# Kernel tuning notes

Measured on AMD Instinct MI355X. Metric: run time of the kernel, lower is better.

## Reference

```python
import jax, jax.numpy as jnp
import numpy as np

TOP_K = 2  # num_experts_per_tok


def setup_inputs() -> dict:
    B, L, D, F, E = 4, 2048, 1024, 2048, 8
    key = jax.random.key(0)
    k0, k1, k2, k3, k4 = jax.random.split(key, 5)
    x = jax.random.normal(k0, (B, L, D), jnp.float32)
    gate_w = jax.random.normal(k1, (D, E), jnp.float32) * 0.02   # router Linear (no bias)
    w1 = jax.random.normal(k2, (E, D, F), jnp.float32) * 0.02    # expert gate proj
    w3 = jax.random.normal(k3, (E, D, F), jnp.float32) * 0.02    # expert up proj
    w2 = jax.random.normal(k4, (E, F, D), jnp.float32) * 0.02    # expert down proj
    return {"x": x, "gate_w": gate_w, "w1": w1, "w3": w3, "w2": w2}


def reference(x, gate_w, w1, w3, w2):
    # ep_size=1: the all_to_all dispatch/return are identities; the math reduces to
    # topk routing -> softmax over selected logits -> per-expert SwiGLU -> weighted combine.
    B, L, D = x.shape
    E = w1.shape[0]
    xf = x.reshape(-1, D)                                  # [N, D]
    N = xf.shape[0]
    router_logits = xf @ gate_w                            # [N, E]
    topk_w, topk_i = jax.lax.top_k(router_logits.astype(jnp.float32), TOP_K)
    topk_w = jax.nn.softmax(topk_w, axis=-1).astype(x.dtype)  # [N, K]
    # Scatter top-k weights into a dense per-expert combine weight [N, E]
    comb = jnp.zeros((N, E), x.dtype)
    comb = comb.at[jnp.arange(N)[:, None], topk_i].add(topk_w)
    # Grouped expert compute: loop over the small fixed expert set, mask-combine.
    out = jnp.zeros_like(xf)
    for e in range(E):
        h = jax.nn.silu(xf @ w1[e]) * (xf @ w3[e])         # [N, F] SwiGLU
        out = out + comb[:, e:e + 1] * (h @ w2[e])         # weighted index_add combine
    return out.reshape(B, L, D), router_logits
```

## Files before the change

### kernel.cpp

```cpp
#include <hip/hip_runtime.h>
#include <hip/hip_bf16.h>

#define DEV __device__ __forceinline__

typedef __attribute__((ext_vector_type(8))) short short8;
typedef __attribute__((ext_vector_type(4))) float f32x4;

constexpr int NTOK = 8192;
constexpr int DIM  = 1024;
constexpr int FF   = 2048;
constexpr int NE   = 8;
constexpr int BM = 128, BN = 128, BK = 64;

DEV void async_copy16(const void* g, void* l) {
  __builtin_amdgcn_global_load_lds(
      (const __attribute__((address_space(1))) unsigned int*)g,
      (__attribute__((address_space(3))) unsigned int*)l, 16, 0, 0);
}

DEV float silu_f(float v) { return v / (1.f + __expf(-v)); }

__global__ void k_convx(const float* __restrict__ x, __hip_bfloat16* __restrict__ xb) {
  size_t i = (size_t)blockIdx.x * blockDim.x + threadIdx.x;
  const float4* s = (const float4*)x + i * 2;
  float4 a = s[0], b = s[1];
  __hip_bfloat16 tmp[8];
  tmp[0] = __float2bfloat16(a.x); tmp[1] = __float2bfloat16(a.y);
  tmp[2] = __float2bfloat16(a.z); tmp[3] = __float2bfloat16(a.w);
  tmp[4] = __float2bfloat16(b.x); tmp[5] = __float2bfloat16(b.y);
  tmp[6] = __float2bfloat16(b.z); tmp[7] = __float2bfloat16(b.w);
  *(short8*)(xb + i * 8) = *(const short8*)tmp;
}

__global__ void k_tconv(const float* __restrict__ src, __hip_bfloat16* __restrict__ dst,
                        int R, int C) {
  const size_t esz = (size_t)R * C;
  src += esz * blockIdx.z;
  dst += esz * blockIdx.z;
  __shared__ float tile[32][33];
  const int t = threadIdx.x;
  const int r0 = blockIdx.y * 32, c0 = blockIdx.x * 32;
#pragma unroll
  for (int i = 0; i < 4; ++i) {
    int lr = i * 8 + (t >> 5), lc = t & 31;
    tile[lr][lc] = src[(size_t)(r0 + lr) * C + c0 + lc];
  }
  __syncthreads();
#pragma unroll
  for (int i = 0; i < 4; ++i) {
    int cc = i * 8 + (t >> 5), rr = t & 31;
    dst[(size_t)(c0 + cc) * R + r0 + rr] = __float2bfloat16(tile[rr][cc]);
  }
}

__global__ void k_router(const float* __restrict__ x, const float* __restrict__ gw,
                         float* __restrict__ logits, int* __restrict__ tok_i,
                         float2* __restrict__ tok_w) {
  const int wave = threadIdx.x >> 6, lane = threadIdx.x & 63;
  const int tok = blockIdx.x * 4 + wave;
  float acc[NE];
#pragma unroll
  for (int e = 0; e < NE; ++e) acc[e] = 0.f;
  const float4* xr = (const float4*)(x + (size_t)tok * DIM);
#pragma unroll
  for (int i = 0; i < DIM / 256; ++i) {
    int d4 = i * 64 + lane;
    float4 xv = xr[d4];
    const float4* g = (const float4*)(gw + (size_t)d4 * 4 * NE);
    float xs[4] = {xv.x, xv.y, xv.z, xv.w};
#pragma unroll
    for (int r = 0; r < 4; ++r) {
      float4 ga = g[r * 2], gb = g[r * 2 + 1];
      acc[0] += xs[r] * ga.x; acc[1] += xs[r] * ga.y;
      acc[2] += xs[r] * ga.z; acc[3] += xs[r] * ga.w;
      acc[4] += xs[r] * gb.x; acc[5] += xs[r] * gb.y;
      acc[6] += xs[r] * gb.z; acc[7] += xs[r] * gb.w;
    }
  }
#pragma unroll
  for (int e = 0; e < NE; ++e) {
#pragma unroll
    for (int off = 32; off; off >>= 1) acc[e] += __shfl_xor(acc[e], off);
  }
  if (lane == 0) {
#pragma unroll
    for (int e = 0; e < NE; ++e) logits[(size_t)tok * NE + e] = acc[e];
    int i0 = 0; float m0 = acc[0];
#pragma unroll
    for (int e = 1; e < NE; ++e) if (acc[e] > m0) { m0 = acc[e]; i0 = e; }
    int i1 = -1; float m1 = -3.4e38f;
#pragma unroll
    for (int e = 0; e < NE; ++e) if (e != i0 && acc[e] > m1) { m1 = acc[e]; i1 = e; }
    float p  = __expf(m1 - m0);
    float wA = 1.f / (1.f + p);
    float wB = p * wA;
    tok_i[tok] = i0 | (i1 << 4);
    tok_w[tok] = make_float2(wA, wB);
  }
}

__global__ void k_place(const int* __restrict__ tok_i, const float2* __restrict__ tok_w,
                        int* __restrict__ slot_token, float* __restrict__ slot_w,
                        int* __restrict__ counts) {
  __shared__ int lcnt[NE], lbase[NE];
  const int t = threadIdx.x;
  const int tok = blockIdx.x * 256 + t;
  if (t < NE) lcnt[t] = 0;
  __syncthreads();
  int pk = tok_i[tok];
  int e0 = pk & 15, e1 = pk >> 4;
  float2 w = tok_w[tok];
  int p0 = atomicAdd(&lcnt[e0], 1);
  int p1 = atomicAdd(&lcnt[e1], 1);
  __syncthreads();
  if (t < NE) lbase[t] = atomicAdd(&counts[t], lcnt[t]);
  __syncthreads();
  int s0 = e0 * NTOK + lbase[e0] + p0;
  slot_token[s0] = tok; slot_w[s0] = w.x;
  int s1 = e1 * NTOK + lbase[e1] + p1;
  slot_token[s1] = tok; slot_w[s1] = w.y;
}

__global__ void k_scan(const int* __restrict__ counts, int* __restrict__ offsets) {
  if (threadIdx.x == 0) {
    int s = 0;
    for (int e = 0; e < NE; ++e) { offsets[e] = s; s += counts[e]; }
  }
}

__global__ __launch_bounds__(256, 2) void k_expert_up(
    const __hip_bfloat16* __restrict__ xb,
    const __hip_bfloat16* __restrict__ w1t,
    const __hip_bfloat16* __restrict__ w3t,
    const int* __restrict__ slot_token, const int* __restrict__ counts,
    const int* __restrict__ offsets,
    __hip_bfloat16* __restrict__ h)
{
  const int e  = blockIdx.z;
  const int cnt = counts[e];
  const int m0 = blockIdx.y * BM;
  if (m0 >= cnt) return;
  const int n0 = blockIdx.x * BN;
  const int tid = threadIdx.x, lane = tid & 63, wave = tid >> 6;
  const int wrow = (wave >> 1) * 64, wcol = (wave & 1) * 64;

  __shared__ __hip_bfloat16 sA[BM * BK];
  __shared__ __hip_bfloat16 sB1[BN * BK];
  __shared__ __hip_bfloat16 sB3[BN * BK];

  const int srow = tid >> 3, scol = tid & 7;
  const int swz = scol ^ (srow & 7);

  const int* stok = slot_token + e * NTOK;
  const __hip_bfloat16* b1e = w1t + (size_t)e * FF * DIM;
  const __hip_bfloat16* b3e = w3t + (size_t)e * FF * DIM;

  const __hip_bfloat16 *gA[4], *gB1[4], *gB3[4];
#pragma unroll
  for (int i = 0; i < 4; ++i) {
    int r = i * 32 + srow;
    int idx = m0 + r;
    int tokv = (idx < cnt) ? stok[idx] : 0;
    gA[i]  = xb  + (size_t)tokv * DIM + swz * 8;
    gB1[i] = b1e + (size_t)(n0 + r) * DIM + swz * 8;
    gB3[i] = b3e + (size_t)(n0 + r) * DIM + swz * 8;
  }
  char* dA  = (char*)sA  + tid * 16;
  char* dB1 = (char*)sB1 + tid * 16;
  char* dB3 = (char*)sB3 + tid * 16;

  f32x4 acc1[4][4], acc3[4][4];
#pragma unroll
  for (int m = 0; m < 4; ++m)
#pragma unroll
    for (int n = 0; n < 4; ++n) { acc1[m][n] = {0, 0, 0, 0}; acc3[m][n] = {0, 0, 0, 0}; }

  for (int kt = 0; kt < DIM / BK; ++kt) {
    const int koff = kt * BK;
#pragma unroll
    for (int i = 0; i < 4; ++i) {
      async_copy16(gA[i]  + koff, dA  + i * 4096);
      async_copy16(gB1[i] + koff, dB1 + i * 4096);
      async_copy16(gB3[i] + koff, dB3 + i * 4096);
    }
    __syncthreads();
#pragma unroll
    for (int kk = 0; kk < 2; ++kk) {
      short8 af[4], b1f[4], b3f[4];
#pragma unroll
      for (int m = 0; m < 4; ++m) {
        int r = wrow + m * 16 + (lane & 15);
        int ch = (kk * 4 + (lane >> 4)) ^ (lane & 7);
        af[m] = *(const short8*)((const char*)sA + r * 128 + ch * 16);
      }
#pragma unroll
      for (int n = 0; n < 4; ++n) {
        int r = wcol + n * 16 + (lane & 15);
        int ch = (kk * 4 + (lane >> 4)) ^ (lane & 7);
        b1f[n] = *(const short8*)((const char*)sB1 + r * 128 + ch * 16);
        b3f[n] = *(const short8*)((const char*)sB3 + r * 128 + ch * 16);
      }
#pragma unroll
      for (int m = 0; m < 4; ++m)
#pragma unroll
        for (int n = 0; n < 4; ++n) {
          acc1[m][n] = __builtin_amdgcn_mfma_f32_16x16x32_bf16(af[m], b1f[n], acc1[m][n], 0, 0, 0);
          acc3[m][n] = __builtin_amdgcn_mfma_f32_16x16x32_bf16(af[m], b3f[n], acc3[m][n], 0, 0, 0);
        }
    }
    __syncthreads();
  }

  const int hb = offsets[e];
#pragma unroll
  for (int m = 0; m < 4; ++m) {
#pragma unroll
    for (int j = 0; j < 4; ++j) {
      int ridx = m0 + wrow + m * 16 + ((lane >> 4) << 2) + j;
      if (ridx < cnt) {
        __hip_bfloat16* hr = h + (size_t)(hb + ridx) * FF + n0 + wcol + (lane & 15);
#pragma unroll
        for (int n = 0; n < 4; ++n) {
          float v1 = acc1[m][n][j], v3 = acc3[m][n][j];
          hr[n * 16] = __float2bfloat16(silu_f(v1) * v3);
        }
      }
    }
  }
}

__global__ __launch_bounds__(256, 2) void k_expert_down(
    const __hip_bfloat16* __restrict__ h,
    const __hip_bfloat16* __restrict__ w2t,
    const int* __restrict__ slot_token, const float* __restrict__ slot_w,
    const int* __restrict__ counts, const int* __restrict__ offsets,
    float* __restrict__ out)
{
  const int e = blockIdx.z;
  const int cnt = counts[e];
  const int m0 = blockIdx.y * BM;
  if (m0 >= cnt) return;
  const int n0 = blockIdx.x * BN;
  const int tid = threadIdx.x, lane = tid & 63, wave = tid >> 6;
  const int wrow = (wave >> 1) * 64, wcol = (wave & 1) * 64;

  __shared__ __hip_bfloat16 sA[BM * BK];
  __shared__ __hip_bfloat16 sB[BN * BK];

  const int srow = tid >> 3, scol = tid & 7;
  const int swz = scol ^ (srow & 7);

  const int hb = offsets[e];
  const __hip_bfloat16* b2e = w2t + (size_t)e * DIM * FF;

  const __hip_bfloat16 *gA[4], *gB[4];
#pragma unroll
  for (int i = 0; i < 4; ++i) {
    int r = i * 32 + srow;
    int idx = m0 + r;
    if (idx >= cnt) idx = 0;
    gA[i] = h   + (size_t)(hb + idx) * FF + swz * 8;
    gB[i] = b2e + (size_t)(n0 + r) * FF + swz * 8;
  }
  char* dA = (char*)sA + tid * 16;
  char* dB = (char*)sB + tid * 16;

  f32x4 acc[4][4];
#pragma unroll
  for (int m = 0; m < 4; ++m)
#pragma unroll
    for (int n = 0; n < 4; ++n) acc[m][n] = {0, 0, 0, 0};

  for (int kt = 0; kt < FF / BK; ++kt) {
    const int koff = kt * BK;
#pragma unroll
    for (int i = 0; i < 4; ++i) {
      async_copy16(gA[i] + koff, dA + i * 4096);
      async_copy16(gB[i] + koff, dB + i * 4096);
    }
    __syncthreads();
#pragma unroll
    for (int kk = 0; kk < 2; ++kk) {
      short8 af[4], bf[4];
#pragma unroll
      for (int m = 0; m < 4; ++m) {
        int r = wrow + m * 16 + (lane & 15);
        int ch = (kk * 4 + (lane >> 4)) ^ (lane & 7);
        af[m] = *(const short8*)((const char*)sA + r * 128 + ch * 16);
      }
#pragma unroll
      for (int n = 0; n < 4; ++n) {
        int r = wcol + n * 16 + (lane & 15);
        int ch = (kk * 4 + (lane >> 4)) ^ (lane & 7);
        bf[n] = *(const short8*)((const char*)sB + r * 128 + ch * 16);
      }
#pragma unroll
      for (int m = 0; m < 4; ++m)
#pragma unroll
        for (int n = 0; n < 4; ++n)
          acc[m][n] = __builtin_amdgcn_mfma_f32_16x16x32_bf16(af[m], bf[n], acc[m][n], 0, 0, 0);
    }
    __syncthreads();
  }

#pragma unroll
  for (int m = 0; m < 4; ++m) {
#pragma unroll
    for (int j = 0; j < 4; ++j) {
      int ridx = m0 + wrow + m * 16 + ((lane >> 4) << 2) + j;
      if (ridx < cnt) {
        int   tok = slot_token[e * NTOK + ridx];
        float wgt = slot_w[e * NTOK + ridx];
        float* orow = out + (size_t)tok * DIM + n0 + wcol + (lane & 15);
#pragma unroll
        for (int n = 0; n < 4; ++n) atomicAdd(&orow[n * 16], wgt * acc[m][n][j]);
      }
    }
  }
}

extern "C" void kernel_launch(void* const* d_in, const int* in_sizes, int n_in,
                              void* d_out, int out_size, void* d_ws, size_t ws_size,
                              hipStream_t stream) {
  const float* x      = (const float*)d_in[0];
  const float* gate_w = (const float*)d_in[1];
  const float* w1     = (const float*)d_in[2];
  const float* w3     = (const float*)d_in[3];
  const float* w2     = (const float*)d_in[4];

  float* out    = (float*)d_out;
  float* logits = out + (size_t)NTOK * DIM;

  char* ws = (char*)d_ws;
  size_t cur = 0;
  auto take = [&](size_t bytes) {
    size_t r = cur;
    cur += (bytes + 255) & ~(size_t)255;
    return r;
  };
  int*    counts     = (int*)(ws + take(32));
  int*    offsets    = (int*)(ws + take(32));
  int*    slot_token = (int*)(ws + take((size_t)NE * NTOK * 4));
  float*  slot_w     = (float*)(ws + take((size_t)NE * NTOK * 4));
  int*    tok_i      = (int*)(ws + take((size_t)NTOK * 4));
  float2* tok_w      = (float2*)(ws + take((size_t)NTOK * 8));
  __hip_bfloat16* xb  = (__hip_bfloat16*)(ws + take((size_t)NTOK * DIM * 2));
  __hip_bfloat16* w1t = (__hip_bfloat16*)(ws + take((size_t)NE * DIM * FF * 2));
  __hip_bfloat16* w3t = (__hip_bfloat16*)(ws + take((size_t)NE * DIM * FF * 2));
  __hip_bfloat16* hbuf = (__hip_bfloat16*)(ws + take((size_t)2 * NTOK * FF * 2));
  __hip_bfloat16* w2t = w1t;

  hipMemsetAsync(counts, 0, 64, stream);
  hipMemsetAsync(out, 0, (size_t)NTOK * DIM * sizeof(float), stream);

  k_convx<<<NTOK * DIM / 8 / 256, 256, 0, stream>>>(x, xb);
  k_tconv<<<dim3(FF / 32, DIM / 32, NE), 256, 0, stream>>>(w1, w1t, DIM, FF);
  k_tconv<<<dim3(FF / 32, DIM / 32, NE), 256, 0, stream>>>(w3, w3t, DIM, FF);
  k_router<<<NTOK / 4, 256, 0, stream>>>(x, gate_w, logits, tok_i, tok_w);
  k_place<<<NTOK / 256, 256, 0, stream>>>(tok_i, tok_w, slot_token, slot_w, counts);
  k_scan<<<1, 64, 0, stream>>>(counts, offsets);
  k_expert_up<<<dim3(FF / BN, NTOK / BM, NE), 256, 0, stream>>>(
      xb, w1t, w3t, slot_token, counts, offsets, hbuf);
  k_tconv<<<dim3(DIM / 32, FF / 32, NE), 256, 0, stream>>>(w2, w2t, FF, DIM);
  k_expert_down<<<dim3(DIM / BN, NTOK / BM, NE), 256, 0, stream>>>(
      hbuf, w2t, slot_token, slot_w, counts, offsets, out);
}
```

Baseline: 573.5 us.

## Replace atomic scatter with staged expert outputs and a gather combine kernel

The down-projection now writes un-weighted per-slot rows to a staging buffer, and a new combine kernel gathers each token's two expert rows and applies the routing weights. This replaces the fp32 atomicAdd scatter and the memset of the output. The bf16 conversion of x is folded into the router kernel, which removes the separate convert kernel. The weight transpose-convert kernel now uses 64x32 tiles with vectorized float4 loads and 16-byte bf16 stores. In exchange there is an extra staging write and read pass, plus workspace aliasing of the stage buffer over xb and w3t, which relies on those buffers being dead by the time the down-projection runs.

```diff
diff --git a/kernel.cpp b/kernel.cpp
--- a/kernel.cpp
+++ b/kernel.cpp
@@ -4,6 +4,7 @@
 #define DEV __device__ __forceinline__
 
 typedef __attribute__((ext_vector_type(8))) short short8;
+typedef __attribute__((ext_vector_type(4))) short short4v;
 typedef __attribute__((ext_vector_type(4))) float f32x4;
 
 constexpr int NTOK = 8192;
@@ -20,42 +21,34 @@
 
 DEV float silu_f(float v) { return v / (1.f + __expf(-v)); }
 
-__global__ void k_convx(const float* __restrict__ x, __hip_bfloat16* __restrict__ xb) {
-  size_t i = (size_t)blockIdx.x * blockDim.x + threadIdx.x;
-  const float4* s = (const float4*)x + i * 2;
-  float4 a = s[0], b = s[1];
-  __hip_bfloat16 tmp[8];
-  tmp[0] = __float2bfloat16(a.x); tmp[1] = __float2bfloat16(a.y);
-  tmp[2] = __float2bfloat16(a.z); tmp[3] = __float2bfloat16(a.w);
-  tmp[4] = __float2bfloat16(b.x); tmp[5] = __float2bfloat16(b.y);
-  tmp[6] = __float2bfloat16(b.z); tmp[7] = __float2bfloat16(b.w);
-  *(short8*)(xb + i * 8) = *(const short8*)tmp;
-}
-
 __global__ void k_tconv(const float* __restrict__ src, __hip_bfloat16* __restrict__ dst,
                         int R, int C) {
   const size_t esz = (size_t)R * C;
   src += esz * blockIdx.z;
   dst += esz * blockIdx.z;
-  __shared__ float tile[32][33];
+  __shared__ float tile[64][33];
   const int t = threadIdx.x;
-  const int r0 = blockIdx.y * 32, c0 = blockIdx.x * 32;
-#pragma unroll
-  for (int i = 0; i < 4; ++i) {
-    int lr = i * 8 + (t >> 5), lc = t & 31;
-    tile[lr][lc] = src[(size_t)(r0 + lr) * C + c0 + lc];
+  const int r0 = blockIdx.y * 64, c0 = blockIdx.x * 32;
+  {
+    int r = t >> 2, cb = (t & 3) * 8;
+    const float4* s = (const float4*)(src + (size_t)(r0 + r) * C + c0 + cb);
+    float4 a = s[0], b = s[1];
+    tile[r][cb + 0] = a.x; tile[r][cb + 1] = a.y; tile[r][cb + 2] = a.z; tile[r][cb + 3] = a.w;
+    tile[r][cb + 4] = b.x; tile[r][cb + 5] = b.y; tile[r][cb + 6] = b.z; tile[r][cb + 7] = b.w;
   }
   __syncthreads();
-#pragma unroll
-  for (int i = 0; i < 4; ++i) {
-    int cc = i * 8 + (t >> 5), rr = t & 31;
-    dst[(size_t)(c0 + cc) * R + r0 + rr] = __float2bfloat16(tile[rr][cc]);
+  {
+    int c = t >> 3, rb = (t & 7) * 8;
+    __hip_bfloat16 tmp[8];
+#pragma unroll
+    for (int k = 0; k < 8; ++k) tmp[k] = __float2bfloat16(tile[rb + k][c]);
+    *(short8*)(dst + (size_t)(c0 + c) * R + r0 + rb) = *(const short8*)tmp;
   }
 }
 
 __global__ void k_router(const float* __restrict__ x, const float* __restrict__ gw,
                          float* __restrict__ logits, int* __restrict__ tok_i,
-                         float2* __restrict__ tok_w) {
+                         float2* __restrict__ tok_w, __hip_bfloat16* __restrict__ xb) {
   const int wave = threadIdx.x >> 6, lane = threadIdx.x & 63;
   const int tok = blockIdx.x * 4 + wave;
   float acc[NE];
@@ -66,6 +59,9 @@
   for (int i = 0; i < DIM / 256; ++i) {
     int d4 = i * 64 + lane;
     float4 xv = xr[d4];
+    __hip_bfloat16 xc[4] = {__float2bfloat16(xv.x), __float2bfloat16(xv.y),
+                            __float2bfloat16(xv.z), __float2bfloat16(xv.w)};
+    *(short4v*)(xb + (size_t)tok * DIM + d4 * 4) = *(const short4v*)xc;
     const float4* g = (const float4*)(gw + (size_t)d4 * 4 * NE);
     float xs[4] = {xv.x, xv.y, xv.z, xv.w};
 #pragma unroll
@@ -99,9 +95,8 @@
   }
 }
 
-__global__ void k_place(const int* __restrict__ tok_i, const float2* __restrict__ tok_w,
-                        int* __restrict__ slot_token, float* __restrict__ slot_w,
-                        int* __restrict__ counts) {
+__global__ void k_place(const int* __restrict__ tok_i, int* __restrict__ slot_token,
+                        int* __restrict__ counts, int2* __restrict__ inv) {
   __shared__ int lcnt[NE], lbase[NE];
   const int t = threadIdx.x;
   const int tok = blockIdx.x * 256 + t;
@@ -109,16 +104,15 @@
   __syncthreads();
   int pk = tok_i[tok];
   int e0 = pk & 15, e1 = pk >> 4;
-  float2 w = tok_w[tok];
   int p0 = atomicAdd(&lcnt[e0], 1);
   int p1 = atomicAdd(&lcnt[e1], 1);
   __syncthreads();
   if (t < NE) lbase[t] = atomicAdd(&counts[t], lcnt[t]);
   __syncthreads();
-  int s0 = e0 * NTOK + lbase[e0] + p0;
-  slot_token[s0] = tok; slot_w[s0] = w.x;
-  int s1 = e1 * NTOK + lbase[e1] + p1;
-  slot_token[s1] = tok; slot_w[s1] = w.y;
+  int g0 = lbase[e0] + p0, g1 = lbase[e1] + p1;
+  slot_token[e0 * NTOK + g0] = tok;
+  slot_token[e1 * NTOK + g1] = tok;
+  inv[tok] = make_int2(e0 * NTOK + g0, e1 * NTOK + g1);
 }
 
 __global__ void k_scan(const int* __restrict__ counts, int* __restrict__ offsets) {
@@ -232,9 +226,8 @@
 __global__ __launch_bounds__(256, 2) void k_expert_down(
     const __hip_bfloat16* __restrict__ h,
     const __hip_bfloat16* __restrict__ w2t,
-    const int* __restrict__ slot_token, const float* __restrict__ slot_w,
     const int* __restrict__ counts, const int* __restrict__ offsets,
-    float* __restrict__ out)
+    float* __restrict__ stage)
 {
   const int e = blockIdx.z;
   const int cnt = counts[e];
@@ -309,14 +302,29 @@
     for (int j = 0; j < 4; ++j) {
       int ridx = m0 + wrow + m * 16 + ((lane >> 4) << 2) + j;
       if (ridx < cnt) {
-        int   tok = slot_token[e * NTOK + ridx];
-        float wgt = slot_w[e * NTOK + ridx];
-        float* orow = out + (size_t)tok * DIM + n0 + wcol + (lane & 15);
-#pragma unroll
-        for (int n = 0; n < 4; ++n) atomicAdd(&orow[n * 16], wgt * acc[m][n][j]);
-      }
-    }
-  }
+        float* sr = stage + (size_t)(hb + ridx) * DIM + n0 + wcol + (lane & 15);
+#pragma unroll
+        for (int n = 0; n < 4; ++n) sr[n * 16] = acc[m][n][j];
+      }
+    }
+  }
+}
+
+__global__ void k_combine(const float* __restrict__ stage, const int2* __restrict__ inv,
+                          const float2* __restrict__ tok_w, const int* __restrict__ offsets,
+                          float* __restrict__ out) {
+  const int tok = blockIdx.x;
+  int2 s = inv[tok];
+  float2 w = tok_w[tok];
+  int r0 = offsets[s.x >> 13] + (s.x & (NTOK - 1));
+  int r1 = offsets[s.y >> 13] + (s.y & (NTOK - 1));
+  const float4* a = (const float4*)(stage + (size_t)r0 * DIM);
+  const float4* b = (const float4*)(stage + (size_t)r1 * DIM);
+  float4* o = (float4*)(out + (size_t)tok * DIM);
+  int c = threadIdx.x;
+  float4 va = a[c], vb = b[c];
+  o[c] = make_float4(w.x * va.x + w.y * vb.x, w.x * va.y + w.y * vb.y,
+                     w.x * va.z + w.y * vb.z, w.x * va.w + w.y * vb.w);
 }
 
 extern "C" void kernel_launch(void* const* d_in, const int* in_sizes, int n_in,
@@ -341,27 +349,29 @@
   int*    counts     = (int*)(ws + take(32));
   int*    offsets    = (int*)(ws + take(32));
   int*    slot_token = (int*)(ws + take((size_t)NE * NTOK * 4));
-  float*  slot_w     = (float*)(ws + take((size_t)NE * NTOK * 4));
   int*    tok_i      = (int*)(ws + take((size_t)NTOK * 4));
   float2* tok_w      = (float2*)(ws + take((size_t)NTOK * 8));
-  __hip_bfloat16* xb  = (__hip_bfloat16*)(ws + take((size_t)NTOK * DIM * 2));
-  __hip_bfloat16* w1t = (__hip_bfloat16*)(ws + take((size_t)NE * DIM * FF * 2));
-  __hip_bfloat16* w3t = (__hip_bfloat16*)(ws + take((size_t)NE * DIM * FF * 2));
+  int2*   inv        = (int2*)(ws + take((size_t)NTOK * 8));
+  __hip_bfloat16* w1t  = (__hip_bfloat16*)(ws + take((size_t)NE * DIM * FF * 2));
+  size_t stage_off = cur;
+  __hip_bfloat16* xb   = (__hip_bfloat16*)(ws + take((size_t)NTOK * DIM * 2));
+  __hip_bfloat16* w3t  = (__hip_bfloat16*)(ws + take((size_t)NE * DIM * FF * 2));
+  (void)take((size_t)NTOK * DIM * 2);
   __hip_bfloat16* hbuf = (__hip_bfloat16*)(ws + take((size_t)2 * NTOK * FF * 2));
-  __hip_bfloat16* w2t = w1t;
+  __hip_bfloat16* w2t  = w1t;
+  float* stage = (float*)(ws + stage_off);
 
   hipMemsetAsync(counts, 0, 64, stream);
-  hipMemsetAsync(out, 0, (size_t)NTOK * DIM * sizeof(float), stream);
-
-  k_convx<<<NTOK * DIM / 8 / 256, 256, 0, stream>>>(x, xb);
-  k_tconv<<<dim3(FF / 32, DIM / 32, NE), 256, 0, stream>>>(w1, w1t, DIM, FF);
-  k_tconv<<<dim3(FF / 32, DIM / 32, NE), 256, 0, stream>>>(w3, w3t, DIM, FF);
-  k_router<<<NTOK / 4, 256, 0, stream>>>(x, gate_w, logits, tok_i, tok_w);
-  k_place<<<NTOK / 256, 256, 0, stream>>>(tok_i, tok_w, slot_token, slot_w, counts);
+
+  k_router<<<NTOK / 4, 256, 0, stream>>>(x, gate_w, logits, tok_i, tok_w, xb);
+  k_place<<<NTOK / 256, 256, 0, stream>>>(tok_i, slot_token, counts, inv);
   k_scan<<<1, 64, 0, stream>>>(counts, offsets);
+  k_tconv<<<dim3(FF / 32, DIM / 64, NE), 256, 0, stream>>>(w1, w1t, DIM, FF);
+  k_tconv<<<dim3(FF / 32, DIM / 64, NE), 256, 0, stream>>>(w3, w3t, DIM, FF);
   k_expert_up<<<dim3(FF / BN, NTOK / BM, NE), 256, 0, stream>>>(
       xb, w1t, w3t, slot_token, counts, offsets, hbuf);
-  k_tconv<<<dim3(DIM / 32, FF / 32, NE), 256, 0, stream>>>(w2, w2t, FF, DIM);
+  k_tconv<<<dim3(DIM / 32, FF / 64, NE), 256, 0, stream>>>(w2, w2t, FF, DIM);
   k_expert_down<<<dim3(DIM / BN, NTOK / BM, NE), 256, 0, stream>>>(
-      hbuf, w2t, slot_token, slot_w, counts, offsets, out);
-}
+      hbuf, w2t, counts, offsets, stage);
+  k_combine<<<NTOK, 256, 0, stream>>>(stage, inv, tok_w, offsets, out);
+}
```

After: 546.1 us. 4.8% less time.
